# Optimization experiments

Measured on AMD Instinct MI355X. Metric: run time of the kernel, lower is better.

Reference implementation:

```python
import jax, jax.numpy as jnp
import numpy as np


def setup_inputs() -> dict:
    key = jax.random.key(0)
    x = jax.random.normal(key, (4, 4096, 4096), dtype=jnp.float32)
    return {"x": x}


def reference(x):
    # Forward of EfficientMemorySiLU: result = F.silu(x).
    # (The per-block quantization / NAIVE compression only affects what is
    #  saved for backward, not the forward output.)
    return x * jax.nn.sigmoid(x)
```

## Files before the change

kernel.cpp:

```cpp
#include <hip/hip_runtime.h>
#include <hip/hip_bf16.h>


__device__ __forceinline__ float silu(float x) {
    return x / (1.0f + __expf(-x));
}

__global__ void __launch_bounds__(256)
silu_fwd_kernel(const float* __restrict__ in, float* __restrict__ out, long long n4) {
    const float4* __restrict__ in4 = (const float4*)in;
    float4* __restrict__ out4 = (float4*)out;

    long long stride = (long long)gridDim.x * blockDim.x;
    for (long long i = (long long)blockIdx.x * blockDim.x + threadIdx.x; i < n4; i += stride) {
        float4 v = in4[i];
        float4 r;
        r.x = silu(v.x);
        r.y = silu(v.y);
        r.z = silu(v.z);
        r.w = silu(v.w);
        out4[i] = r;
    }
}

__global__ void silu_fwd_tail_kernel(const float* __restrict__ in, float* __restrict__ out,
                                     long long start, long long n) {
    long long i = start + blockIdx.x * blockDim.x + threadIdx.x;
    if (i < n) out[i] = silu(in[i]);
}

extern "C" void kernel_launch(void* const* d_in, const int* in_sizes, int n_in,
                              void* d_out, int out_size, void* d_ws, size_t ws_size,
                              hipStream_t stream) {
    const float* x = (const float*)d_in[0];
    float* out = (float*)d_out;
    long long n = (long long)in_sizes[0];

    long long n4 = n / 4;
    const int block = 256;
    long long want = (n4 + block - 1) / block;
    int grid = (int)(want < 2048 ? want : 2048);
    if (grid < 1) grid = 1;

    silu_fwd_kernel<<<grid, block, 0, stream>>>(x, out, n4);

    long long rem = n - n4 * 4;
    if (rem > 0) {
        int tgrid = (int)((rem + block - 1) / block);
        silu_fwd_tail_kernel<<<tgrid, block, 0, stream>>>(x, out, n4 * 4, n);
    }
}
```

Baseline: 428.2 us.

## Use one-shot blocks with nontemporal stores and fast exp2/rcp SiLU

Replaces the capped grid-stride loop with a non-looping grid in which each thread handles two float4 vectors. Output is written with nontemporal stores so the streamed results do not pollute the cache. The sigmoid now uses the hardware exp2 and reciprocal intrinsics instead of __expf and a division. This trades a small loss of accuracy from the approximate reciprocal and launches many more blocks.

```diff
diff --git a/kernel.cpp b/kernel.cpp
--- a/kernel.cpp
+++ b/kernel.cpp
@@ -2,31 +2,38 @@
 #include <hip/hip_bf16.h>
 
 
-__device__ __forceinline__ float silu(float x) {
-    return x / (1.0f + __expf(-x));
+typedef float f32x4 __attribute__((ext_vector_type(4)));
+
+__device__ __forceinline__ float silu_fast(float x) {
+    const float LOG2E = 1.4426950408889634f;
+    float t = __builtin_amdgcn_exp2f(-x * LOG2E);
+    return x * __builtin_amdgcn_rcpf(1.0f + t);
+}
+
+__device__ __forceinline__ f32x4 silu4(f32x4 v) {
+    f32x4 r;
+    r.x = silu_fast(v.x);
+    r.y = silu_fast(v.y);
+    r.z = silu_fast(v.z);
+    r.w = silu_fast(v.w);
+    return r;
 }
 
 __global__ void __launch_bounds__(256)
-silu_fwd_kernel(const float* __restrict__ in, float* __restrict__ out, long long n4) {
-    const float4* __restrict__ in4 = (const float4*)in;
-    float4* __restrict__ out4 = (float4*)out;
-
-    long long stride = (long long)gridDim.x * blockDim.x;
-    for (long long i = (long long)blockIdx.x * blockDim.x + threadIdx.x; i < n4; i += stride) {
-        float4 v = in4[i];
-        float4 r;
-        r.x = silu(v.x);
-        r.y = silu(v.y);
-        r.z = silu(v.z);
-        r.w = silu(v.w);
-        out4[i] = r;
-    }
+silu_fwd_kernel(const f32x4* __restrict__ in, f32x4* __restrict__ out) {
+    long long base = (long long)blockIdx.x * 512 + threadIdx.x;
+    f32x4 a = in[base];
+    f32x4 b = in[base + 256];
+    f32x4 ra = silu4(a);
+    f32x4 rb = silu4(b);
+    __builtin_nontemporal_store(ra, &out[base]);
+    __builtin_nontemporal_store(rb, &out[base + 256]);
 }
 
 __global__ void silu_fwd_tail_kernel(const float* __restrict__ in, float* __restrict__ out,
                                      long long start, long long n) {
-    long long i = start + blockIdx.x * blockDim.x + threadIdx.x;
-    if (i < n) out[i] = silu(in[i]);
+    long long i = start + (long long)blockIdx.x * blockDim.x + threadIdx.x;
+    if (i < n) out[i] = silu_fast(in[i]);
 }
 
 extern "C" void kernel_launch(void* const* d_in, const int* in_sizes, int n_in,
@@ -37,16 +44,15 @@
     long long n = (long long)in_sizes[0];
 
     long long n4 = n / 4;
-    const int block = 256;
-    long long want = (n4 + block - 1) / block;
-    int grid = (int)(want < 2048 ? want : 2048);
-    if (grid < 1) grid = 1;
-
-    silu_fwd_kernel<<<grid, block, 0, stream>>>(x, out, n4);
-
-    long long rem = n - n4 * 4;
+    long long blocks = n4 / 512;
+    if (blocks > 0) {
+        silu_fwd_kernel<<<(int)blocks, 256, 0, stream>>>(
+            (const f32x4*)x, (f32x4*)out);
+    }
+    long long done = blocks * 512 * 4;
+    long long rem = n - done;
     if (rem > 0) {
-        int tgrid = (int)((rem + block - 1) / block);
-        silu_fwd_tail_kernel<<<tgrid, block, 0, stream>>>(x, out, n4 * 4, n);
+        int tgrid = (int)((rem + 255) / 256);
+        silu_fwd_tail_kernel<<<tgrid, 256, 0, stream>>>(x, out, done, n);
     }
 }
```

Result: slower. 437.5 us (+2.2%).
